# Performance work log

Hardware: AMD Instinct MI355X
Metric: run time of the kernel (lower is better)

## Reference

```python
import jax, jax.numpy as jnp
import numpy as np

B, T, C, H = 8, 1024, 1024, 16  # batch, seq, n_embd, n_head


def setup_inputs() -> dict:
    key = jax.random.key(0)
    ks = jax.random.split(key, 5)
    scale = 1.0 / np.sqrt(C)
    return {
        "x": jax.random.normal(ks[0], (B, T, C), dtype=jnp.float32),
        "Wqkv": jax.random.normal(ks[1], (C, 3 * C), dtype=jnp.float32) * scale,
        "bqkv": jax.random.normal(ks[2], (3 * C,), dtype=jnp.float32) * 0.02,
        "Wproj": jax.random.normal(ks[3], (C, C), dtype=jnp.float32) * scale,
        "bproj": jax.random.normal(ks[4], (C,), dtype=jnp.float32) * 0.02,
        "n_head": H,
    }


def reference(x, Wqkv, bqkv, Wproj, bproj, n_head):
    Bb, Tt, Cc = x.shape
    hd = Cc // n_head  # head dim
    qkv = x @ Wqkv + bqkv                      # [B,T,3C]
    q, k, v = jnp.split(qkv, 3, axis=-1)       # each [B,T,C]
    # [B,T,C] -> [B,H,T,hd]
    def to_heads(t):
        return t.reshape(Bb, Tt, n_head, hd).transpose(0, 2, 1, 3)
    q, k, v = to_heads(q), to_heads(k), to_heads(v)
    scores = jnp.einsum("bhqd,bhkd->bhqk", q, k) / jnp.sqrt(jnp.asarray(hd, q.dtype))
    causal = jnp.tril(jnp.ones((Tt, Tt), dtype=bool))
    scores = jnp.where(causal, scores, jnp.asarray(-jnp.inf, scores.dtype))
    attn = jax.nn.softmax(scores, axis=-1)
    y = jnp.einsum("bhqk,bhkd->bhqd", attn, v)  # [B,H,T,hd]
    y = y.transpose(0, 2, 1, 3).reshape(Bb, Tt, Cc)
    return y @ Wproj + bproj
```

## Files before the change

kernel.cpp:

```cpp
#include <hip/hip_runtime.h>
#include <hip/hip_bf16.h>
#include <math.h>
#include <type_traits>

#define Bz 8
#define Tz 1024
#define Cz 1024
#define Hz 16
#define HDz 64
#define Mz (Bz*Tz)
#define N1 (3*Cz)
#define QKN 2048

typedef __attribute__((ext_vector_type(8))) short short8;
typedef __attribute__((ext_vector_type(4))) short short4v;
typedef __attribute__((ext_vector_type(4))) float floatx4;

__device__ __forceinline__ unsigned short f2bf(float f) {
    unsigned u = __float_as_uint(f);
    return (unsigned short)((u + 0x7FFFu + ((u >> 16) & 1u)) >> 16);
}

__device__ __forceinline__ unsigned pkbf(float a, float b) {
    __hip_bfloat162 h = __float22bfloat162_rn(make_float2(a, b));
    return *(unsigned*)&h;
}

__device__ __forceinline__ void gload16(const void* g, void* l) {
    __builtin_amdgcn_global_load_lds(
        (const __attribute__((address_space(1))) unsigned int*)g,
        (__attribute__((address_space(3))) unsigned int*)l, 16, 0, 0);
}

__global__ __launch_bounds__(256) void prep_kernel(
    const float* __restrict__ x, unsigned short* __restrict__ xb,
    const float* __restrict__ Wqkv, unsigned short* __restrict__ Wqkvt,
    const float* __restrict__ Wproj, unsigned short* __restrict__ Wprojt)
{
    __shared__ float tile[32][33];
    const int bid = blockIdx.x;
    const int tid = threadIdx.x;
    if (bid < 8192) {
        int i = bid * 256 + tid;
        float4 v = *(const float4*)&x[(size_t)i * 4];
        ushort4 o;
        o.x = f2bf(v.x); o.y = f2bf(v.y); o.z = f2bf(v.z); o.w = f2bf(v.w);
        *(ushort4*)&xb[(size_t)i * 4] = o;
        return;
    }
    const float* W; unsigned short* Wt; int K, N, n0, k0;
    if (bid < 11264) {
        int b = bid - 8192;  W = Wqkv;  Wt = Wqkvt;  K = Cz; N = N1;
        n0 = (b % 96) * 32;  k0 = (b / 96) * 32;
    } else {
        int b = bid - 11264; W = Wproj; Wt = Wprojt; K = Cz; N = Cz;
        n0 = (b % 32) * 32;  k0 = (b / 32) * 32;
    }
    const int tx = tid & 31, ty = tid >> 5;
#pragma unroll
    for (int i = 0; i < 4; ++i)
        tile[ty + i * 8][tx] = W[(size_t)(k0 + ty + i * 8) * N + n0 + tx];
    __syncthreads();
#pragma unroll
    for (int i = 0; i < 4; ++i)
        Wt[(size_t)(n0 + ty + i * 8) * K + k0 + tx] = f2bf(tile[tx][ty + i * 8]);
}

__global__ __launch_bounds__(256) void gemm_kernel(const unsigned short* __restrict__ A,
    const unsigned short* __restrict__ Bt, const float* __restrict__ bias,
    void* __restrict__ Cout, unsigned short* __restrict__ VtG,
    int M, int N, int K, int mode)
{
    __shared__ unsigned short As[128 * 64];
    __shared__ unsigned short Bs[128 * 64];
    const int tid = threadIdx.x;
    const int lane = tid & 63;
    const int w = tid >> 6, wr = w >> 1, wc = w & 1;
    const int quad = lane >> 4, m16 = lane & 15;
    const int row0 = blockIdx.y * 128, col0 = blockIdx.x * 128;

    float bv[4];
#pragma unroll
    for (int ni = 0; ni < 4; ++ni)
        bv[ni] = bias[col0 + wc * 64 + ni * 16 + m16];

    floatx4 acc[4][4];
#pragma unroll
    for (int mi = 0; mi < 4; ++mi)
#pragma unroll
        for (int ni = 0; ni < 4; ++ni)
            acc[mi][ni] = (floatx4){0.f, 0.f, 0.f, 0.f};

    const int l3 = lane >> 3;
    const int swz = ((lane & 7) ^ l3) * 8;
    const unsigned short* gA[4];
    const unsigned short* gB[4];
    unsigned short* lA[4];
    unsigned short* lB[4];
#pragma unroll
    for (int i = 0; i < 4; ++i) {
        int c = w * 4 + i;
        gA[i] = A  + (size_t)(row0 + c * 8 + l3) * K + swz;
        gB[i] = Bt + (size_t)(col0 + c * 8 + l3) * K + swz;
        lA[i] = &As[c * 512];
        lB[i] = &Bs[c * 512];
    }
    const int sw7 = m16 & 7;

    for (int k0 = 0; k0 < K; k0 += 64) {
#pragma unroll
        for (int i = 0; i < 4; ++i) {
            gload16(gA[i] + k0, lA[i]);
            gload16(gB[i] + k0, lB[i]);
        }
        __syncthreads();
#pragma unroll
        for (int s = 0; s < 2; ++s) {
            short8 af[4], bfr[4];
            const int ch = ((s * 4 + quad) ^ sw7) * 8;
#pragma unroll
            for (int mi = 0; mi < 4; ++mi)
                af[mi] = *(short8*)&As[(wr * 64 + mi * 16 + m16) * 64 + ch];
#pragma unroll
            for (int ni = 0; ni < 4; ++ni)
                bfr[ni] = *(short8*)&Bs[(wc * 64 + ni * 16 + m16) * 64 + ch];
#pragma unroll
            for (int mi = 0; mi < 4; ++mi)
#pragma unroll
                for (int ni = 0; ni < 4; ++ni)
                    acc[mi][ni] = __builtin_amdgcn_mfma_f32_16x16x32_bf16(af[mi], bfr[ni], acc[mi][ni], 0, 0, 0);
        }
        __syncthreads();
    }

    if (mode == 0) {
#pragma unroll
        for (int mi = 0; mi < 4; ++mi)
#pragma unroll
            for (int ni = 0; ni < 4; ++ni)
#pragma unroll
                for (int reg = 0; reg < 4; ++reg) {
                    int r = row0 + wr * 64 + mi * 16 + quad * 4 + reg;
                    int c = col0 + wc * 64 + ni * 16 + m16;
                    ((float*)Cout)[(size_t)r * N + c] = acc[mi][ni][reg] + bv[ni];
                }
    }
}

__global__ __launch_bounds__(512) void gemm256_qkv(const unsigned short* __restrict__ A,
    const unsigned short* __restrict__ Bt, const float* __restrict__ bias,
    unsigned short* __restrict__ Cqk, unsigned short* __restrict__ VtG)
{
    __shared__ unsigned short lds[2 * 2 * 2 * 8192];
    constexpr int NT = 16;

    const int tid = threadIdx.x;
    const int lane = tid & 63;
    const int w = tid >> 6;
    const int wm = w >> 2, wn = w & 3;
    const int quad = lane >> 4, m16 = lane & 15;
    const int sw7 = m16 & 7;

    int wg = blockIdx.x;
    wg = (wg & 7) * 48 + (wg >> 3);
    const int bx = wg % 12, by = wg / 12;
    const int row0 = by * 256, col0 = bx * 256;

    const int srow = tid >> 3;
    const int scol = ((tid & 7) ^ (srow & 7)) * 8;
    const unsigned short* sA[2][2];
    const unsigned short* sB[2][2];
#pragma unroll
    for (int h = 0; h < 2; ++h)
#pragma unroll
        for (int c = 0; c < 2; ++c) {
            sA[h][c] = A  + (size_t)(row0 + h * 128 + c * 64 + srow) * Cz + scol;
            sB[h][c] = Bt + (size_t)(col0 + h * 128 + c * 64 + srow) * Cz + scol;
        }

    auto stage = [&](int mat, int h, int kt, int db) {
        const unsigned short* s0 = (mat ? sB[h][0] : sA[h][0]) + kt * 64;
        const unsigned short* s1 = (mat ? sB[h][1] : sA[h][1]) + kt * 64;
        unsigned short* d = &lds[db * 32768 + mat * 16384 + h * 8192 + w * 512];
        gload16(s0, d);
        gload16(s1, d + 4096);
    };

    float bv[4];
#pragma unroll
    for (int ni = 0; ni < 4; ++ni)
        bv[ni] = bias[col0 + wn * 64 + ni * 16 + m16];

    floatx4 acc[8][4];
#pragma unroll
    for (int mi = 0; mi < 8; ++mi)
#pragma unroll
        for (int ni = 0; ni < 4; ++ni)
            acc[mi][ni] = (floatx4){0.f, 0.f, 0.f, 0.f};

    stage(1, 0, 0, 0); stage(1, 1, 0, 0); stage(0, 0, 0, 0); stage(0, 1, 0, 0);
    stage(1, 0, 1, 1); stage(1, 1, 1, 1); stage(0, 0, 1, 1);
    asm volatile("s_waitcnt vmcnt(6)" ::: "memory");
    __builtin_amdgcn_s_barrier();

    const int rB0 = ((wn & 1) * 64 + m16) * 64;
    const int lBoff = 16384 + (wn >> 1) * 8192;

    auto tile_step = [&](const int b, const int kt) {
        const unsigned short* lA = &lds[b * 32768];
        const unsigned short* lB = &lds[b * 32768 + lBoff];
        short8 bfr[4][2];
#pragma unroll
        for (int p = 0; p < 4; ++p) {
            const int hf = p >> 1;
            short8 af[2][2];
#pragma unroll
            for (int j = 0; j < 2; ++j) {
                const int ra = ((p & 1) * 64 + j * 32 + wm * 16 + m16) * 64;
#pragma unroll
                for (int ks = 0; ks < 2; ++ks)
                    af[j][ks] = *(const short8*)&lA[hf * 8192 + ra + ((((ks << 2) | quad) ^ sw7) << 3)];
            }
            if (p == 0) {
#pragma unroll
                for (int ni = 0; ni < 4; ++ni)
#pragma unroll
                    for (int ks = 0; ks < 2; ++ks)
                        bfr[ni][ks] = *(const short8*)&lB[rB0 + ni * 1024 + ((((ks << 2) | quad) ^ sw7) << 3)];
                if (kt + 1 < NT) stage(0, 1, kt + 1, b ^ 1);
            } else if (kt + 2 < NT) {
                if (p == 1)      stage(1, 0, kt + 2, b);
                else if (p == 2) stage(1, 1, kt + 2, b);
                else             stage(0, 0, kt + 2, b);
            }
            __builtin_amdgcn_s_barrier();
            asm volatile("s_waitcnt lgkmcnt(0)" ::: "memory");
            __builtin_amdgcn_sched_barrier(0);
            __builtin_amdgcn_s_setprio(1);
#pragma unroll
            for (int ks = 0; ks < 2; ++ks)
#pragma unroll
                for (int j = 0; j < 2; ++j)
#pragma unroll
                    for (int ni = 0; ni < 4; ++ni)
                        acc[p * 2 + j][ni] = __builtin_amdgcn_mfma_f32_16x16x32_bf16(
                            af[j][ks], bfr[ni][ks], acc[p * 2 + j][ni], 0, 0, 0);
            __builtin_amdgcn_s_setprio(0);
            if (p == 3) {
                if (kt < NT - 2) { asm volatile("s_waitcnt vmcnt(6)" ::: "memory"); }
                else             { asm volatile("s_waitcnt vmcnt(0)" ::: "memory"); }
            }
            __builtin_amdgcn_s_barrier();
        }
    };

#pragma unroll 1
    for (int j = 0; j < 7; ++j) {
        tile_step(0, 2 * j);
        tile_step(1, 2 * j + 1);
    }
    tile_step(0, 14);
    tile_step(1, 15);

    if (bx < 8) {
#pragma unroll
        for (int mi = 0; mi < 8; ++mi)
#pragma unroll
            for (int ni = 0; ni < 4; ++ni) {
                const int c = col0 + wn * 64 + ni * 16 + m16;
#pragma unroll
                for (int reg = 0; reg < 4; ++reg) {
                    const int r = row0 + mi * 32 + wm * 16 + quad * 4 + reg;
                    Cqk[(size_t)r * QKN + c] = f2bf(acc[mi][ni][reg] + bv[ni]);
                }
            }
    } else {
        const int hsel = (bx - 8) * 4 + wn;
        const int bq = row0 >> 10;
        const int tb = row0 & 1023;
#pragma unroll
        for (int ni = 0; ni < 4; ++ni) {
            const int dd = ni * 16 + m16;
            unsigned short* drow = VtG
                + (size_t)(bq * Hz + hsel) * (HDz * Tz)
                + (size_t)dd * Tz + tb;
#pragma unroll
            for (int mi = 0; mi < 8; ++mi) {
                const int t = mi * 32 + wm * 16 + quad * 4;
                unsigned pk[2];
                pk[0] = pkbf(acc[mi][ni][0] + bv[ni], acc[mi][ni][1] + bv[ni]);
                pk[1] = pkbf(acc[mi][ni][2] + bv[ni], acc[mi][ni][3] + bv[ni]);
                *(uint2*)&drow[t] = *(uint2*)pk;
            }
        }
    }
}

__global__ __launch_bounds__(128) void attn_kernel(const unsigned short* __restrict__ qkb,
    const unsigned short* __restrict__ VtG, unsigned short* __restrict__ attb)
{
    __shared__ unsigned short Ks[2][64 * 64];
    __shared__ unsigned short Vs[2][64 * 64];

    const int bx = blockIdx.x;
    const int bh = blockIdx.y;
    const int b = bh >> 4, h = bh & 15;
    const int tid = threadIdx.x, lane = tid & 63, w = tid >> 6;
    const int quad = lane >> 4, m16 = lane & 15;
    const int qis[2] = {15 - bx, bx};

    const unsigned short* Kb = qkb + (size_t)(b * Tz) * QKN + Cz + h * HDz;
    const unsigned short* Vb = VtG + (size_t)bh * (HDz * Tz);

    const int l3 = lane >> 3, l7 = lane & 7;
    const int gsw = ((l7 ^ l3) << 3);
    const int sw = m16 & 7;
    const int p0 = (quad ^ sw) << 3;

    short8 onesf = (short8){0,0,0,0,0,0,0,0};
    if (m16 == 0) {
        const short one = (short)0x3F80;
        onesf = (short8){one,one,one,one,one,one,one,one};
    }

    int srow[4];
#pragma unroll
    for (int i = 0; i < 4; ++i) srow[i] = w * 32 + i * 8 + l3;

#pragma unroll
    for (int i = 0; i < 4; ++i) {
        gload16(Kb + (size_t)srow[i] * QKN + gsw, &Ks[0][(w * 4 + i) * 512]);
        gload16(Vb + (size_t)srow[i] * Tz + gsw, &Vs[0][(w * 4 + i) * 512]);
    }

    int buf = 0;
    for (int t = 0; t < 2; ++t) {
        const int qi = qis[t];

        short8 qf[2][2];
        int qrow[2];
#pragma unroll
        for (int mi = 0; mi < 2; ++mi) {
            qrow[mi] = qi * 64 + w * 32 + mi * 16 + m16;
            const size_t rq = (size_t)(b * Tz + qrow[mi]) * QKN + h * HDz;
            qf[mi][0] = *(const short8*)&qkb[rq + quad * 8];
            qf[mi][1] = *(const short8*)&qkb[rq + 32 + quad * 8];
        }

        floatx4 of[2][4];
#pragma unroll
        for (int mi = 0; mi < 2; ++mi)
#pragma unroll
            for (int dc = 0; dc < 4; ++dc) of[mi][dc] = (floatx4){0.f, 0.f, 0.f, 0.f};
        floatx4 lsum[2];
        lsum[0] = (floatx4){0.f, 0.f, 0.f, 0.f};
        lsum[1] = (floatx4){0.f, 0.f, 0.f, 0.f};

        auto tile_body = [&](auto diag_c) {
            constexpr bool DIAG = decltype(diag_c)::value;
            short8 pf[2][2];
#pragma unroll
            for (int m0 = 0; m0 < 4; ++m0) {
                if (DIAG && w == 0 && m0 >= 2) continue;
                const unsigned short* kr = &Ks[buf][(m0 * 16 + m16) * 64];
                short8 kf0 = *(const short8*)&kr[p0];
                short8 kf1 = *(const short8*)&kr[p0 ^ 32];
#pragma unroll
                for (int mi = 0; mi < 2; ++mi) {
                    floatx4 st = (floatx4){0.f, 0.f, 0.f, 0.f};
                    st = __builtin_amdgcn_mfma_f32_16x16x32_bf16(kf0, qf[mi][0], st, 0, 0, 0);
                    st = __builtin_amdgcn_mfma_f32_16x16x32_bf16(kf1, qf[mi][1], st, 0, 0, 0);
                    float p[4];
#pragma unroll
                    for (int reg = 0; reg < 4; ++reg) {
                        p[reg] = exp2f(st[reg] * 0.18033688f);
                        if (DIAG) {
                            int key = m0 * 16 + quad * 4 + reg;
                            int qr  = w * 32 + mi * 16 + m16;
                            p[reg] = (key <= qr) ? p[reg] : 0.f;
                        }
                    }
                    unsigned* pp = (unsigned*)&pf[mi][m0 >> 1];
                    pp[(m0 & 1) * 2 + 0] = pkbf(p[0], p[1]);
                    pp[(m0 & 1) * 2 + 1] = pkbf(p[2], p[3]);
                }
            }
#pragma unroll
            for (int kg = 0; kg < 2; ++kg) {
                if (DIAG && w == 0 && kg == 1) continue;
#pragma unroll
                for (int mi = 0; mi < 2; ++mi)
                    lsum[mi] = __builtin_amdgcn_mfma_f32_16x16x32_bf16(onesf, pf[mi][kg], lsum[mi], 0, 0, 0);
#pragma unroll
                for (int dc = 0; dc < 4; ++dc) {
                    const unsigned short* vrow = &Vs[buf][(dc * 16 + m16) * 64];
                    const int g0 = kg * 4 + (quad >> 1);
                    const int off = (quad & 1) * 4;
                    short4v v0 = *(const short4v*)&vrow[((g0 ^ sw) << 3) + off];
                    short4v v1 = *(const short4v*)&vrow[(((g0 + 2) ^ sw) << 3) + off];
                    short8 vf;
                    vf[0] = v0[0]; vf[1] = v0[1]; vf[2] = v0[2]; vf[3] = v0[3];
                    vf[4] = v1[0]; vf[5] = v1[1]; vf[6] = v1[2]; vf[7] = v1[3];
#pragma unroll
                    for (int mi = 0; mi < 2; ++mi)
                        of[mi][dc] = __builtin_amdgcn_mfma_f32_16x16x32_bf16(vf, pf[mi][kg], of[mi][dc], 0, 0, 0);
                }
            }
        };

        for (int ki = 0; ki <= qi; ++ki) {
            __syncthreads();
            const int nk = (ki < qi) ? (ki + 1) : (t == 0 ? 0 : -1);
            if (nk >= 0) {
                const size_t ko = (size_t)nk * 64;
#pragma unroll
                for (int i = 0; i < 4; ++i) {
                    gload16(Kb + (ko + srow[i]) * QKN + gsw, &Ks[buf ^ 1][(w * 4 + i) * 512]);
                    gload16(Vb + (size_t)srow[i] * Tz + ko + gsw, &Vs[buf ^ 1][(w * 4 + i) * 512]);
                }
            }
            if (ki == qi) tile_body(std::true_type{});
            else          tile_body(std::false_type{});
            buf ^= 1;
        }

#pragma unroll
        for (int mi = 0; mi < 2; ++mi) {
            const float l = __shfl(lsum[mi][0], m16);
            const float inv = 1.f / l;
            const size_t orow = (size_t)(b * Tz + qrow[mi]) * Cz + h * HDz;
#pragma unroll
            for (int dc = 0; dc < 4; ++dc) {
                ushort4 o;
                o.x = f2bf(of[mi][dc][0] * inv);
                o.y = f2bf(of[mi][dc][1] * inv);
                o.z = f2bf(of[mi][dc][2] * inv);
                o.w = f2bf(of[mi][dc][3] * inv);
                *(ushort4*)&attb[orow + dc * 16 + quad * 4] = o;
            }
        }
    }
}

extern "C" void kernel_launch(void* const* d_in, const int* in_sizes, int n_in,
                              void* d_out, int out_size, void* d_ws, size_t ws_size,
                              hipStream_t stream)
{
    const float* x     = (const float*)d_in[0];
    const float* Wqkv  = (const float*)d_in[1];
    const float* bqkv  = (const float*)d_in[2];
    const float* Wproj = (const float*)d_in[3];
    const float* bproj = (const float*)d_in[4];
    float* out = (float*)d_out;

    unsigned short* xb     = (unsigned short*)d_ws;
    unsigned short* Wqkvt  = xb + (size_t)Mz * Cz;
    unsigned short* Wprojt = Wqkvt + (size_t)N1 * Cz;
    unsigned short* qkb    = Wprojt + (size_t)Cz * Cz;
    unsigned short* VtG    = qkb + (size_t)Mz * QKN;
    unsigned short* attb   = xb;

    prep_kernel<<<12288, 256, 0, stream>>>(x, xb, Wqkv, Wqkvt, Wproj, Wprojt);

    gemm256_qkv<<<(N1 / 256) * (Mz / 256), 512, 0, stream>>>(
        xb, Wqkvt, bqkv, qkb, VtG);

    attn_kernel<<<dim3(8, Bz * Hz), 128, 0, stream>>>(qkb, VtG, attb);

    gemm_kernel<<<dim3(Cz / 128, Mz / 128), 256, 0, stream>>>(
        attb, Wprojt, bproj, out, nullptr, Mz, Cz, Cz, 0);
}
```

Before: 249.9 us.

## Retile QKV GEMM to 256x192 tiles for balanced 512-block grid

Changes the QKV GEMM tile from 256x256 to 256x192 so the grid becomes 512 workgroups instead of 384. The aim is to remove the partial-wave tail imbalance across the GPU's compute units. It restructures LDS layout, the B staging into three 64-row chunks, the vmcnt waits, and the epilogue's QK/V split per 16-column fragment. In exchange, each tile has lower arithmetic intensity, with more A reloads per output column.

```diff
diff --git a/kernel.cpp b/kernel.cpp
--- a/kernel.cpp
+++ b/kernel.cpp
@@ -151,7 +151,7 @@
     const unsigned short* __restrict__ Bt, const float* __restrict__ bias,
     unsigned short* __restrict__ Cqk, unsigned short* __restrict__ VtG)
 {
-    __shared__ unsigned short lds[2 * 2 * 2 * 8192];
+    __shared__ unsigned short lds[2 * 28672];
     constexpr int NT = 16;
 
     const int tid = threadIdx.x;
@@ -162,54 +162,55 @@
     const int sw7 = m16 & 7;
 
     int wg = blockIdx.x;
-    wg = (wg & 7) * 48 + (wg >> 3);
-    const int bx = wg % 12, by = wg / 12;
-    const int row0 = by * 256, col0 = bx * 256;
+    wg = (wg & 7) * 64 + (wg >> 3);
+    const int bx = wg % 16, by = wg / 16;
+    const int row0 = by * 256, col0 = bx * 192;
 
     const int srow = tid >> 3;
     const int scol = ((tid & 7) ^ (srow & 7)) * 8;
     const unsigned short* sA[2][2];
-    const unsigned short* sB[2][2];
+    const unsigned short* sB3[3];
 #pragma unroll
     for (int h = 0; h < 2; ++h)
 #pragma unroll
-        for (int c = 0; c < 2; ++c) {
-            sA[h][c] = A  + (size_t)(row0 + h * 128 + c * 64 + srow) * Cz + scol;
-            sB[h][c] = Bt + (size_t)(col0 + h * 128 + c * 64 + srow) * Cz + scol;
-        }
-
-    auto stage = [&](int mat, int h, int kt, int db) {
-        const unsigned short* s0 = (mat ? sB[h][0] : sA[h][0]) + kt * 64;
-        const unsigned short* s1 = (mat ? sB[h][1] : sA[h][1]) + kt * 64;
-        unsigned short* d = &lds[db * 32768 + mat * 16384 + h * 8192 + w * 512];
-        gload16(s0, d);
-        gload16(s1, d + 4096);
+        for (int c = 0; c < 2; ++c)
+            sA[h][c] = A + (size_t)(row0 + h * 128 + c * 64 + srow) * Cz + scol;
+#pragma unroll
+    for (int u = 0; u < 3; ++u)
+        sB3[u] = Bt + (size_t)(col0 + u * 64 + srow) * Cz + scol;
+
+    auto stageA = [&](int h, int kt, int db) {
+        unsigned short* d = &lds[db * 28672 + h * 8192 + w * 512];
+        gload16(sA[h][0] + kt * 64, d);
+        gload16(sA[h][1] + kt * 64, d + 4096);
     };
-
-    float bv[4];
-#pragma unroll
-    for (int ni = 0; ni < 4; ++ni)
-        bv[ni] = bias[col0 + wn * 64 + ni * 16 + m16];
-
-    floatx4 acc[8][4];
+    auto stageB = [&](int u, int kt, int db) {
+        gload16(sB3[u] + kt * 64, &lds[db * 28672 + 16384 + u * 4096 + w * 512]);
+    };
+
+    float bv[3];
+#pragma unroll
+    for (int ni = 0; ni < 3; ++ni)
+        bv[ni] = bias[col0 + wn * 48 + ni * 16 + m16];
+
+    floatx4 acc[8][3];
 #pragma unroll
     for (int mi = 0; mi < 8; ++mi)
 #pragma unroll
-        for (int ni = 0; ni < 4; ++ni)
+        for (int ni = 0; ni < 3; ++ni)
             acc[mi][ni] = (floatx4){0.f, 0.f, 0.f, 0.f};
 
-    stage(1, 0, 0, 0); stage(1, 1, 0, 0); stage(0, 0, 0, 0); stage(0, 1, 0, 0);
-    stage(1, 0, 1, 1); stage(1, 1, 1, 1); stage(0, 0, 1, 1);
-    asm volatile("s_waitcnt vmcnt(6)" ::: "memory");
-    __builtin_amdgcn_s_barrier();
-
-    const int rB0 = ((wn & 1) * 64 + m16) * 64;
-    const int lBoff = 16384 + (wn >> 1) * 8192;
+    stageB(0, 0, 0); stageB(1, 0, 0); stageB(2, 0, 0);
+    stageA(0, 0, 0); stageA(1, 0, 0);
+    stageB(0, 1, 1); stageB(1, 1, 1); stageB(2, 1, 1);
+    stageA(0, 1, 1);
+    asm volatile("s_waitcnt vmcnt(5)" ::: "memory");
+    asm volatile("s_barrier" ::: "memory");
 
     auto tile_step = [&](const int b, const int kt) {
-        const unsigned short* lA = &lds[b * 32768];
-        const unsigned short* lB = &lds[b * 32768 + lBoff];
-        short8 bfr[4][2];
+        const unsigned short* lA = &lds[b * 28672];
+        const unsigned short* lB = &lds[b * 28672 + 16384];
+        short8 bfr[3][2];
 #pragma unroll
         for (int p = 0; p < 4; ++p) {
             const int hf = p >> 1;
@@ -223,17 +224,19 @@
             }
             if (p == 0) {
 #pragma unroll
-                for (int ni = 0; ni < 4; ++ni)
+                for (int ni = 0; ni < 3; ++ni) {
+                    const int rb = (wn * 48 + ni * 16 + m16) * 64;
 #pragma unroll
                     for (int ks = 0; ks < 2; ++ks)
-                        bfr[ni][ks] = *(const short8*)&lB[rB0 + ni * 1024 + ((((ks << 2) | quad) ^ sw7) << 3)];
-                if (kt + 1 < NT) stage(0, 1, kt + 1, b ^ 1);
+                        bfr[ni][ks] = *(const short8*)&lB[rb + ((((ks << 2) | quad) ^ sw7) << 3)];
+                }
+                if (kt + 1 < NT) stageA(1, kt + 1, b ^ 1);
             } else if (kt + 2 < NT) {
-                if (p == 1)      stage(1, 0, kt + 2, b);
-                else if (p == 2) stage(1, 1, kt + 2, b);
-                else             stage(0, 0, kt + 2, b);
-            }
-            __builtin_amdgcn_s_barrier();
+                if (p == 1)      { stageB(0, kt + 2, b); stageB(1, kt + 2, b); }
+                else if (p == 2) { stageB(2, kt + 2, b); }
+                else             { stageA(0, kt + 2, b); }
+            }
+            asm volatile("s_barrier" ::: "memory");
             asm volatile("s_waitcnt lgkmcnt(0)" ::: "memory");
             __builtin_amdgcn_sched_barrier(0);
             __builtin_amdgcn_s_setprio(1);
@@ -242,15 +245,15 @@
 #pragma unroll
                 for (int j = 0; j < 2; ++j)
 #pragma unroll
-                    for (int ni = 0; ni < 4; ++ni)
+                    for (int ni = 0; ni < 3; ++ni)
                         acc[p * 2 + j][ni] = __builtin_amdgcn_mfma_f32_16x16x32_bf16(
                             af[j][ks], bfr[ni][ks], acc[p * 2 + j][ni], 0, 0, 0);
             __builtin_amdgcn_s_setprio(0);
             if (p == 3) {
-                if (kt < NT - 2) { asm volatile("s_waitcnt vmcnt(6)" ::: "memory"); }
+                if (kt < NT - 2) { asm volatile("s_waitcnt vmcnt(5)" ::: "memory"); }
                 else             { asm volatile("s_waitcnt vmcnt(0)" ::: "memory"); }
             }
-            __builtin_amdgcn_s_barrier();
+            asm volatile("s_barrier" ::: "memory");
         }
     };
 
@@ -262,25 +265,23 @@
     tile_step(0, 14);
     tile_step(1, 15);
 
-    if (bx < 8) {
-#pragma unroll
-        for (int mi = 0; mi < 8; ++mi)
-#pragma unroll
-            for (int ni = 0; ni < 4; ++ni) {
-                const int c = col0 + wn * 64 + ni * 16 + m16;
+#pragma unroll
+    for (int ni = 0; ni < 3; ++ni) {
+        const int c0 = col0 + wn * 48 + ni * 16;
+        if (c0 < 2048) {
+#pragma unroll
+            for (int mi = 0; mi < 8; ++mi)
 #pragma unroll
                 for (int reg = 0; reg < 4; ++reg) {
                     const int r = row0 + mi * 32 + wm * 16 + quad * 4 + reg;
-                    Cqk[(size_t)r * QKN + c] = f2bf(acc[mi][ni][reg] + bv[ni]);
-                }
-            }
-    } else {
-        const int hsel = (bx - 8) * 4 + wn;
-        const int bq = row0 >> 10;
-        const int tb = row0 & 1023;
-#pragma unroll
-        for (int ni = 0; ni < 4; ++ni) {
-            const int dd = ni * 16 + m16;
+                    Cqk[(size_t)r * QKN + c0 + m16] = f2bf(acc[mi][ni][reg] + bv[ni]);
+                }
+        } else {
+            const int cb = c0 - 2048;
+            const int hsel = cb >> 6;
+            const int dd = (cb & 63) + m16;
+            const int bq = row0 >> 10;
+            const int tb = row0 & 1023;
             unsigned short* drow = VtG
                 + (size_t)(bq * Hz + hsel) * (HDz * Tz)
                 + (size_t)dd * Tz + tb;
@@ -462,8 +463,7 @@
 
     prep_kernel<<<12288, 256, 0, stream>>>(x, xb, Wqkv, Wqkvt, Wproj, Wprojt);
 
-    gemm256_qkv<<<(N1 / 256) * (Mz / 256), 512, 0, stream>>>(
-        xb, Wqkvt, bqkv, qkb, VtG);
+    gemm256_qkv<<<512, 512, 0, stream>>>(xb, Wqkvt, bqkv, qkb, VtG);
 
     attn_kernel<<<dim3(8, Bz * Hz), 128, 0, stream>>>(qkb, VtG, attb);
 
```

After: 240.4 us. 3.8% less time.
